# Performance work log

Measured on AMD Instinct MI355X. Metric: run time of the kernel, lower is better.

## Reference

```python
import jax, jax.numpy as jnp
import numpy as np

N_NODES = 50000
N_EDGES = 1600000
D_FEAT = 32
SCALE = 1.0
EPS = 1e-12


def setup_inputs() -> dict:
    key = jax.random.key(0)
    k1, k2 = jax.random.split(key)
    x = jax.random.normal(k1, (N_NODES, D_FEAT), dtype=jnp.float32)
    edge_index = jax.random.randint(k2, (2, N_EDGES), 0, N_NODES, dtype=jnp.int32)
    return {"x": x, "edge_index": edge_index}


def reference(x, edge_index):
    index_i = edge_index[0]  # target nodes (segments)
    index_j = edge_index[1]  # source nodes (gathered)

    # in-degree per target node, clamped to 1 (torch_scatter 'mean' semantics:
    # empty segments get mean 0)
    ones = jnp.ones((index_i.shape[0],), dtype=x.dtype)
    deg = jax.ops.segment_sum(ones, index_i, num_segments=N_NODES)
    deg = jnp.maximum(deg, 1.0)[:, None]  # [N, 1]

    # neighborhood mean of features
    mean = jax.ops.segment_sum(x[index_j], index_i, num_segments=N_NODES) / deg

    # neighborhood mean of squared deviations -> std
    reduced_x = (x - mean) ** 2
    var = jax.ops.segment_sum(reduced_x[index_j], index_i, num_segments=N_NODES) / deg
    std = jnp.sqrt(var + EPS)

    out = SCALE * x / std
    # replace infs with the original x, as in the torch module
    out = jnp.where(jnp.isinf(out), x, out)
    return out
```

## Files before the change

### kernel.cpp

```cpp
#include <hip/hip_runtime.h>
#include <hip/hip_fp16.h>
#include <math.h>

#define DF 32
#define EPSF 1e-12f
#define PB 128
#define PB_SHIFT 7
#define NBMAX 512
#define CAP 5120
#define CHUNK 4096
#define EPT 16

__global__ __launch_bounds__(256) void k_passA(
    const int* __restrict__ ii, const int* __restrict__ jj,
    const float* __restrict__ x, int* __restrict__ gcount,
    unsigned int* __restrict__ bucketed, __half* __restrict__ xh,
    int ne, int nb, int nfeat) {
  __shared__ int hist[NBMAX];
  __shared__ int histc[NBMAX];
  __shared__ int bb[NBMAX];
  __shared__ int excl_s[NBMAX];
  __shared__ int sc[256];
  __shared__ unsigned int stage[CHUNK];
  int t = threadIdx.x;
  hist[t] = 0; hist[t + 256] = 0;
  __syncthreads();

  int base = blockIdx.x * CHUNK;
  unsigned int pk[EPT];
  int rk[EPT];
#pragma unroll
  for (int k = 0; k < EPT; ++k) {
    int e = base + t + k * 256;
    if (e < ne) {
      int i = ii[e], j = jj[e];
      int b = i >> PB_SHIFT;
      pk[k] = ((unsigned)b << 23) | ((unsigned)(i & (PB - 1)) << 16) | (unsigned)j;
      rk[k] = atomicAdd(&hist[b], 1);
    } else {
      rk[k] = -1;
    }
  }

  {
    int base8 = blockIdx.x * (CHUNK / 8);
#pragma unroll
    for (int r = 0; r < 2; ++r) {
      int p8 = base8 + r * 256 + t;
      if (p8 * 8 < nfeat) {
        float4 a = ((const float4*)x)[2 * p8];
        float4 bq = ((const float4*)x)[2 * p8 + 1];
        union { __half2 h[4]; float4 f; } u;
        u.h[0] = __floats2half2_rn(a.x, a.y);
        u.h[1] = __floats2half2_rn(a.z, a.w);
        u.h[2] = __floats2half2_rn(bq.x, bq.y);
        u.h[3] = __floats2half2_rn(bq.z, bq.w);
        ((float4*)xh)[p8] = u.f;
      }
    }
  }
  __syncthreads();
  histc[t] = hist[t]; histc[t + 256] = hist[t + 256];
  __syncthreads();
#pragma unroll
  for (int b = t; b < NBMAX; b += 256) {
    int c = histc[b];
    bb[b] = (b < nb && c > 0) ? atomicAdd(&gcount[b], c) : 0;
  }
  int a0 = histc[2 * t], a1 = histc[2 * t + 1];
  sc[t] = a0 + a1;
  __syncthreads();
  int pv = sc[t];
  for (int s = 1; s < 256; s <<= 1) {
    int v = 0;
    if (t >= s) v = sc[t - s];
    __syncthreads();
    if (t >= s) sc[t] += v;
    __syncthreads();
  }
  int eP = sc[t] - pv;
  excl_s[2 * t] = eP;
  excl_s[2 * t + 1] = eP + a0;
  __syncthreads();
#pragma unroll
  for (int k = 0; k < EPT; ++k) {
    if (rk[k] >= 0) {
      int b = pk[k] >> 23;
      stage[excl_s[b] + rk[k]] = pk[k];
    }
  }
  __syncthreads();
  int bcnt = ne - base;
  if (bcnt > CHUNK) bcnt = CHUNK;
  for (int p = t; p < bcnt; p += 256) {
    unsigned int v = stage[p];
    int b = v >> 23;
    bucketed[(size_t)b * CAP + bb[b] + (p - excl_s[b])] = v;
  }
}

__global__ __launch_bounds__(256) void k_passB(
    const unsigned int* __restrict__ bucketed, const int* __restrict__ gcount,
    int* __restrict__ sortedj, int* __restrict__ deg_g, int* __restrict__ curend_g,
    int* __restrict__ perm, int n_nodes, int nb) {
  __shared__ int sc[256];
  __shared__ int lh[PB];
  __shared__ int lcur[PB];
  __shared__ int dh[PB];
  __shared__ int dcur[PB];
  __shared__ int sgbase;
  int b = blockIdx.x;
  int t = threadIdx.x;

  int g0 = (2 * t < nb) ? gcount[2 * t] : 0;
  int g1 = (2 * t + 1 < nb) ? gcount[2 * t + 1] : 0;
  sc[t] = g0 + g1;
  __syncthreads();
  int pv = sc[t];
  for (int s = 1; s < 256; s <<= 1) {
    int v = 0;
    if (t >= s) v = sc[t - s];
    __syncthreads();
    if (t >= s) sc[t] += v;
    __syncthreads();
  }
  if (2 * t == b) sgbase = sc[t] - pv;
  if (2 * t + 1 == b) sgbase = sc[t] - pv + g0;
  if (t < PB) { lh[t] = 0; dh[t] = 0; }
  __syncthreads();
  int gbase = sgbase;
  int cnt = gcount[b];

  const unsigned int* src = bucketed + (size_t)b * CAP;
  for (int p = t; p < cnt; p += 256) {
    int il = (src[p] >> 16) & (PB - 1);
    atomicAdd(&lh[il], 1);
  }
  __syncthreads();
  int a = (t < PB) ? lh[t] : 0;
  if (t < PB) sc[t] = a;
  __syncthreads();
  for (int s = 1; s < PB; s <<= 1) {
    int v = 0;
    if (t < PB && t >= s) v = sc[t - s];
    __syncthreads();
    if (t < PB && t >= s) sc[t] += v;
    __syncthreads();
  }
  int excl = (t < PB) ? sc[t] - a : 0;
  int node = b * PB + t;
  bool nvalid = (t < PB) && (node < n_nodes);
  if (t < PB) lcur[t] = excl;
  if (nvalid) {
    deg_g[node] = a;
    curend_g[node] = gbase + excl + a;
    atomicAdd(&dh[a < PB - 1 ? a : PB - 1], 1);
  }
  __syncthreads();
  int d0 = (t < PB) ? dh[t] : 0;
  if (t < PB) sc[t] = d0;
  __syncthreads();
  for (int s = 1; s < PB; s <<= 1) {
    int v = 0;
    if (t < PB && t >= s) v = sc[t - s];
    __syncthreads();
    if (t < PB && t >= s) sc[t] += v;
    __syncthreads();
  }
  if (t < PB) dcur[t] = sc[t] - d0;
  __syncthreads();
  if (nvalid) {
    int bin = a < PB - 1 ? a : PB - 1;
    int pos = atomicAdd(&dcur[bin], 1);
    perm[b * PB + pos] = node;
  } else if (t < PB) {
    perm[b * PB + t] = -1;
  }
  __syncthreads();
  for (int p = t; p < cnt; p += 256) {
    unsigned int v = src[p];
    int il = (v >> 16) & (PB - 1);
    int pos = atomicAdd(&lcur[il], 1);
    sortedj[gbase + pos] = (int)(v & 0xFFFFu);
  }
}

__global__ __launch_bounds__(256) void k_meansq(
    const int* __restrict__ perm, const int* __restrict__ sortedj,
    const int* __restrict__ curend, const int* __restrict__ deg,
    const __half* __restrict__ xh, const float* __restrict__ x,
    __half* __restrict__ yh, int nperm) {
  int wv = (int)((blockIdx.x * blockDim.x + threadIdx.x) >> 6);
  int lane = threadIdx.x & 63;
  int g = lane >> 3;
  int r = (lane >> 2) & 1;
  int c = lane & 3;
  int ni = wv * 8 + g;
  int w = perm[ni];
  bool valid = (w >= 0);
  int dg = valid ? deg[w] : 0;
  int end = valid ? curend[w] : 0;
  int start = end - dg;
  int co = c * 8;
  __half2 aA0 = {}, aA1 = {}, aA2 = {}, aA3 = {};
  __half2 aB0 = {}, aB1 = {}, aB2 = {}, aB3 = {};
  int s = start + r;
  for (; s + 6 < end; s += 8) {
    int j0 = sortedj[s], j1 = sortedj[s + 2], j2 = sortedj[s + 4], j3 = sortedj[s + 6];
    float4 v0 = *(const float4*)&xh[j0 * DF + co];
    float4 v1 = *(const float4*)&xh[j1 * DF + co];
    float4 v2 = *(const float4*)&xh[j2 * DF + co];
    float4 v3 = *(const float4*)&xh[j3 * DF + co];
    const __half2* h0 = (const __half2*)&v0;
    const __half2* h1 = (const __half2*)&v1;
    const __half2* h2 = (const __half2*)&v2;
    const __half2* h3 = (const __half2*)&v3;
    aA0 = __hadd2(aA0, h0[0]); aA1 = __hadd2(aA1, h0[1]);
    aA2 = __hadd2(aA2, h0[2]); aA3 = __hadd2(aA3, h0[3]);
    aB0 = __hadd2(aB0, h1[0]); aB1 = __hadd2(aB1, h1[1]);
    aB2 = __hadd2(aB2, h1[2]); aB3 = __hadd2(aB3, h1[3]);
    aA0 = __hadd2(aA0, h2[0]); aA1 = __hadd2(aA1, h2[1]);
    aA2 = __hadd2(aA2, h2[2]); aA3 = __hadd2(aA3, h2[3]);
    aB0 = __hadd2(aB0, h3[0]); aB1 = __hadd2(aB1, h3[1]);
    aB2 = __hadd2(aB2, h3[2]); aB3 = __hadd2(aB3, h3[3]);
  }
  for (; s < end; s += 2) {
    int j = sortedj[s];
    float4 v = *(const float4*)&xh[j * DF + co];
    const __half2* h = (const __half2*)&v;
    aA0 = __hadd2(aA0, h[0]); aA1 = __hadd2(aA1, h[1]);
    aA2 = __hadd2(aA2, h[2]); aA3 = __hadd2(aA3, h[3]);
  }
  __half2 s0 = __hadd2(aA0, aB0), s1 = __hadd2(aA1, aB1);
  __half2 s2 = __hadd2(aA2, aB2), s3 = __hadd2(aA3, aB3);
  union { __half2 h; int i; } u0, u1, u2, u3;
  u0.h = s0; u1.h = s1; u2.h = s2; u3.h = s3;
  u0.i = __shfl_xor(u0.i, 4); s0 = __hadd2(s0, u0.h);
  u1.i = __shfl_xor(u1.i, 4); s1 = __hadd2(s1, u1.h);
  u2.i = __shfl_xor(u2.i, 4); s2 = __hadd2(s2, u2.h);
  u3.i = __shfl_xor(u3.i, 4); s3 = __hadd2(s3, u3.h);
  if (valid && r == 0) {
    float inv = 1.0f / fmaxf((float)dg, 1.0f);
    float2 m0 = __half22float2(s0);
    float2 m1 = __half22float2(s1);
    float2 m2 = __half22float2(s2);
    float2 m3 = __half22float2(s3);
    float4 xa = *(const float4*)&x[w * DF + co];
    float4 xb = *(const float4*)&x[w * DF + co + 4];
    float d0 = xa.x - m0.x * inv;
    float d1 = xa.y - m0.y * inv;
    float d2 = xa.z - m1.x * inv;
    float d3 = xa.w - m1.y * inv;
    float d4 = xb.x - m2.x * inv;
    float d5 = xb.y - m2.y * inv;
    float d6 = xb.z - m3.x * inv;
    float d7 = xb.w - m3.y * inv;
    union { __half2 h[4]; float4 f; } uo;
    uo.h[0] = __floats2half2_rn(d0 * d0, d1 * d1);
    uo.h[1] = __floats2half2_rn(d2 * d2, d3 * d3);
    uo.h[2] = __floats2half2_rn(d4 * d4, d5 * d5);
    uo.h[3] = __floats2half2_rn(d6 * d6, d7 * d7);
    *(float4*)&yh[w * DF + co] = uo.f;
  }
}

__global__ __launch_bounds__(256) void k_varfinal(
    const int* __restrict__ perm, const int* __restrict__ sortedj,
    const int* __restrict__ curend, const int* __restrict__ deg,
    const __half* __restrict__ yh, const float* __restrict__ x,
    float* __restrict__ out, int nperm) {
  int wv = (int)((blockIdx.x * blockDim.x + threadIdx.x) >> 6);
  int lane = threadIdx.x & 63;
  int g = lane >> 3;
  int r = (lane >> 2) & 1;
  int c = lane & 3;
  int ni = wv * 8 + g;
  int w = perm[ni];
  bool valid = (w >= 0);
  int dg = valid ? deg[w] : 0;
  int end = valid ? curend[w] : 0;
  int start = end - dg;
  int co = c * 8;
  float accA[8], accB[8];
#pragma unroll
  for (int k = 0; k < 8; ++k) { accA[k] = 0.f; accB[k] = 0.f; }
  int s = start + r;
  for (; s + 6 < end; s += 8) {
    int j0 = sortedj[s], j1 = sortedj[s + 2], j2 = sortedj[s + 4], j3 = sortedj[s + 6];
    float4 v0 = *(const float4*)&yh[j0 * DF + co];
    float4 v1 = *(const float4*)&yh[j1 * DF + co];
    float4 v2 = *(const float4*)&yh[j2 * DF + co];
    float4 v3 = *(const float4*)&yh[j3 * DF + co];
    const __half2* h0 = (const __half2*)&v0;
    const __half2* h1 = (const __half2*)&v1;
    const __half2* h2 = (const __half2*)&v2;
    const __half2* h3 = (const __half2*)&v3;
#pragma unroll
    for (int k = 0; k < 4; ++k) {
      float2 f0 = __half22float2(h0[k]);
      float2 f1 = __half22float2(h1[k]);
      float2 f2 = __half22float2(h2[k]);
      float2 f3 = __half22float2(h3[k]);
      accA[2 * k]     += f0.x + f2.x;
      accA[2 * k + 1] += f0.y + f2.y;
      accB[2 * k]     += f1.x + f3.x;
      accB[2 * k + 1] += f1.y + f3.y;
    }
  }
  for (; s < end; s += 2) {
    int j = sortedj[s];
    float4 v = *(const float4*)&yh[j * DF + co];
    const __half2* h = (const __half2*)&v;
#pragma unroll
    for (int k = 0; k < 4; ++k) {
      float2 f = __half22float2(h[k]);
      accA[2 * k]     += f.x;
      accA[2 * k + 1] += f.y;
    }
  }
  float acc[8];
#pragma unroll
  for (int k = 0; k < 8; ++k) {
    acc[k] = accA[k] + accB[k];
    acc[k] += __shfl_xor(acc[k], 4);
  }
  if (valid && r == 0) {
    float dgc = fmaxf((float)dg, 1.0f);
    float4 xa = *(const float4*)&x[w * DF + co];
    float4 xb = *(const float4*)&x[w * DF + co + 4];
    float xs[8] = {xa.x, xa.y, xa.z, xa.w, xb.x, xb.y, xb.z, xb.w};
    float o[8];
#pragma unroll
    for (int k = 0; k < 8; ++k) {
      float sq = sqrtf(acc[k] / dgc + EPSF);
      o[k] = xs[k] / sq;
      if (isinf(o[k])) o[k] = xs[k];
    }
    float4 oa = {o[0], o[1], o[2], o[3]};
    float4 ob = {o[4], o[5], o[6], o[7]};
    *(float4*)&out[w * DF + co] = oa;
    *(float4*)&out[w * DF + co + 4] = ob;
  }
}

extern "C" void kernel_launch(void* const* d_in, const int* in_sizes, int n_in,
                              void* d_out, int out_size, void* d_ws, size_t ws_size,
                              hipStream_t stream) {
  const float* x = (const float*)d_in[0];
  const int* ei = (const int*)d_in[1];
  const int n_nodes = in_sizes[0] / DF;
  const int ne = in_sizes[1] / 2;
  const int* ii = ei;
  const int* jj = ei + ne;
  const int nb = (n_nodes + PB - 1) / PB;
  const int nfeat = n_nodes * DF;
  const int nperm = nb * PB;

  char* wsb = (char*)d_ws;
  size_t off = 0;
  auto align16 = [](size_t v) { return (v + 15) & ~(size_t)15; };
  int* gcount = (int*)(wsb + off); off = align16(off + NBMAX * 4);
  int* deg    = (int*)(wsb + off); off = align16(off + (size_t)n_nodes * 4);
  int* curend = (int*)(wsb + off); off = align16(off + (size_t)n_nodes * 4);
  int* perm   = (int*)(wsb + off); off = align16(off + (size_t)nperm * 4);
  int* sortedj= (int*)(wsb + off); off = align16(off + (size_t)ne * 4);
  unsigned int* bucketed = (unsigned int*)(wsb + off);
  off = align16(off + (size_t)nb * CAP * 4);
  __half* xh = (__half*)(wsb + off); off = align16(off + (size_t)nfeat * 2);
  __half* yh = (__half*)(wsb + off);

  float* out = (float*)d_out;

  hipMemsetAsync(gcount, 0, NBMAX * sizeof(int), stream);

  int nblkA = (ne + CHUNK - 1) / CHUNK;
  int nblkF = (nfeat + CHUNK - 1) / CHUNK;
  if (nblkF > nblkA) nblkA = nblkF;
  k_passA<<<nblkA, 256, 0, stream>>>(ii, jj, x, gcount, bucketed, xh, ne, nb, nfeat);
  k_passB<<<nb, 256, 0, stream>>>(bucketed, gcount, sortedj, deg, curend, perm, n_nodes, nb);

  int gblocks = nperm / 32;
  k_meansq<<<gblocks, 256, 0, stream>>>(perm, sortedj, curend, deg, xh, x, yh, nperm);
  k_varfinal<<<gblocks, 256, 0, stream>>>(perm, sortedj, curend, deg, yh, x, out, nperm);
}
```

Before: 85.77 us.

## Drop LDS staging in bucketing pass and write scattered directly with smaller chunks

Pass A no longer sorts each chunk's packed edges into a shared-memory staging buffer with a block-wide prefix scan before writing them out. Each edge is now written straight to its global bucket slot from registers. The chunk size is halved so twice as many blocks run, each with less work and much less shared memory. This removes the scan, several barriers and the LDS round trip, at the cost of less coalesced global writes and twice as many global atomics on the bucket counters.

```diff
diff --git a/kernel.cpp b/kernel.cpp
--- a/kernel.cpp
+++ b/kernel.cpp
@@ -8,8 +8,8 @@
 #define PB_SHIFT 7
 #define NBMAX 512
 #define CAP 5120
-#define CHUNK 4096
-#define EPT 16
+#define CHUNK 2048
+#define EPT 8
 
 __global__ __launch_bounds__(256) void k_passA(
     const int* __restrict__ ii, const int* __restrict__ jj,
@@ -17,11 +17,7 @@
     unsigned int* __restrict__ bucketed, __half* __restrict__ xh,
     int ne, int nb, int nfeat) {
   __shared__ int hist[NBMAX];
-  __shared__ int histc[NBMAX];
   __shared__ int bb[NBMAX];
-  __shared__ int excl_s[NBMAX];
-  __shared__ int sc[256];
-  __shared__ unsigned int stage[CHUNK];
   int t = threadIdx.x;
   hist[t] = 0; hist[t + 256] = 0;
   __syncthreads();
@@ -43,59 +39,31 @@
   }
 
   {
-    int base8 = blockIdx.x * (CHUNK / 8);
-#pragma unroll
-    for (int r = 0; r < 2; ++r) {
-      int p8 = base8 + r * 256 + t;
-      if (p8 * 8 < nfeat) {
-        float4 a = ((const float4*)x)[2 * p8];
-        float4 bq = ((const float4*)x)[2 * p8 + 1];
-        union { __half2 h[4]; float4 f; } u;
-        u.h[0] = __floats2half2_rn(a.x, a.y);
-        u.h[1] = __floats2half2_rn(a.z, a.w);
-        u.h[2] = __floats2half2_rn(bq.x, bq.y);
-        u.h[3] = __floats2half2_rn(bq.z, bq.w);
-        ((float4*)xh)[p8] = u.f;
-      }
-    }
-  }
-  __syncthreads();
-  histc[t] = hist[t]; histc[t + 256] = hist[t + 256];
+    int p8 = blockIdx.x * (CHUNK / 8) + t;
+    if (p8 * 8 < nfeat) {
+      float4 a = ((const float4*)x)[2 * p8];
+      float4 bq = ((const float4*)x)[2 * p8 + 1];
+      union { __half2 h[4]; float4 f; } u;
+      u.h[0] = __floats2half2_rn(a.x, a.y);
+      u.h[1] = __floats2half2_rn(a.z, a.w);
+      u.h[2] = __floats2half2_rn(bq.x, bq.y);
+      u.h[3] = __floats2half2_rn(bq.z, bq.w);
+      ((float4*)xh)[p8] = u.f;
+    }
+  }
   __syncthreads();
 #pragma unroll
   for (int b = t; b < NBMAX; b += 256) {
-    int c = histc[b];
+    int c = hist[b];
     bb[b] = (b < nb && c > 0) ? atomicAdd(&gcount[b], c) : 0;
   }
-  int a0 = histc[2 * t], a1 = histc[2 * t + 1];
-  sc[t] = a0 + a1;
-  __syncthreads();
-  int pv = sc[t];
-  for (int s = 1; s < 256; s <<= 1) {
-    int v = 0;
-    if (t >= s) v = sc[t - s];
-    __syncthreads();
-    if (t >= s) sc[t] += v;
-    __syncthreads();
-  }
-  int eP = sc[t] - pv;
-  excl_s[2 * t] = eP;
-  excl_s[2 * t + 1] = eP + a0;
   __syncthreads();
 #pragma unroll
   for (int k = 0; k < EPT; ++k) {
     if (rk[k] >= 0) {
       int b = pk[k] >> 23;
-      stage[excl_s[b] + rk[k]] = pk[k];
-    }
-  }
-  __syncthreads();
-  int bcnt = ne - base;
-  if (bcnt > CHUNK) bcnt = CHUNK;
-  for (int p = t; p < bcnt; p += 256) {
-    unsigned int v = stage[p];
-    int b = v >> 23;
-    bucketed[(size_t)b * CAP + bb[b] + (p - excl_s[b])] = v;
+      bucketed[(size_t)b * CAP + bb[b] + rk[k]] = pk[k];
+    }
   }
 }
 
```

Result: slower. 97.42 us (+13.6%).

## Fuse bucket sort with neighbor-mean pass and store sorted indices as ushort

Applied to the files above, without the earlier changes.

Merges the per-bucket counting sort kernel with the mean and squared-deviation gather kernel. The sorted source indices are kept in LDS and the mean is computed in the same block, which removes one kernel launch and the global round-trip of the sorted index list for the mean pass. The global sorted index array also shrinks to 16-bit entries for the variance pass. In exchange, the gather now runs in only one block per 128-node bucket rather than many small blocks, so there are fewer waves in flight to hide gather latency, and the larger LDS footprint may lower occupancy.

```diff
diff --git a/kernel.cpp b/kernel.cpp
--- a/kernel.cpp
+++ b/kernel.cpp
@@ -95,22 +95,28 @@
   for (int p = t; p < bcnt; p += 256) {
     unsigned int v = stage[p];
     int b = v >> 23;
-    bucketed[(size_t)b * CAP + bb[b] + (p - excl_s[b])] = v;
+    int excl = excl_s[b];
+    bucketed[(size_t)b * CAP + bb[b] + (p - excl)] = v;
   }
 }
 
-__global__ __launch_bounds__(256) void k_passB(
+__global__ __launch_bounds__(256) void k_sortmean(
     const unsigned int* __restrict__ bucketed, const int* __restrict__ gcount,
-    int* __restrict__ sortedj, int* __restrict__ deg_g, int* __restrict__ curend_g,
-    int* __restrict__ perm, int n_nodes, int nb) {
+    const __half* __restrict__ xh, const float* __restrict__ x,
+    __half* __restrict__ yh, unsigned short* __restrict__ sortedj,
+    int* __restrict__ deg_g, int* __restrict__ curend_g, int* __restrict__ perm,
+    int n_nodes, int nb) {
   __shared__ int sc[256];
   __shared__ int lh[PB];
   __shared__ int lcur[PB];
   __shared__ int dh[PB];
   __shared__ int dcur[PB];
+  __shared__ int nstart[PB];
+  __shared__ int ndeg[PB];
+  __shared__ int npl[PB];
+  __shared__ unsigned short sjl[CAP];
   __shared__ int sgbase;
-  int b = blockIdx.x;
-  int t = threadIdx.x;
+  int b = blockIdx.x, t = threadIdx.x;
 
   int g0 = (2 * t < nb) ? gcount[2 * t] : 0;
   int g1 = (2 * t + 1 < nb) ? gcount[2 * t + 1] : 0;
@@ -130,12 +136,9 @@
   __syncthreads();
   int gbase = sgbase;
   int cnt = gcount[b];
-
   const unsigned int* src = bucketed + (size_t)b * CAP;
-  for (int p = t; p < cnt; p += 256) {
-    int il = (src[p] >> 16) & (PB - 1);
-    atomicAdd(&lh[il], 1);
-  }
+
+  for (int p = t; p < cnt; p += 256) atomicAdd(&lh[(src[p] >> 16) & (PB - 1)], 1);
   __syncthreads();
   int a = (t < PB) ? lh[t] : 0;
   if (t < PB) sc[t] = a;
@@ -150,7 +153,7 @@
   int excl = (t < PB) ? sc[t] - a : 0;
   int node = b * PB + t;
   bool nvalid = (t < PB) && (node < n_nodes);
-  if (t < PB) lcur[t] = excl;
+  if (t < PB) { lcur[t] = excl; nstart[t] = excl; ndeg[t] = a; }
   if (nvalid) {
     deg_g[node] = a;
     curend_g[node] = gbase + excl + a;
@@ -172,8 +175,10 @@
   if (nvalid) {
     int bin = a < PB - 1 ? a : PB - 1;
     int pos = atomicAdd(&dcur[bin], 1);
+    npl[pos] = t;
     perm[b * PB + pos] = node;
   } else if (t < PB) {
+    npl[t] = -1;
     perm[b * PB + t] = -1;
   }
   __syncthreads();
@@ -181,91 +186,88 @@
     unsigned int v = src[p];
     int il = (v >> 16) & (PB - 1);
     int pos = atomicAdd(&lcur[il], 1);
-    sortedj[gbase + pos] = (int)(v & 0xFFFFu);
+    sjl[pos] = (unsigned short)(v & 0xFFFFu);
+  }
+  __syncthreads();
+  for (int p = t; p < cnt; p += 256) sortedj[gbase + p] = sjl[p];
+
+  int wvl = t >> 6, lane = t & 63;
+  int g = lane >> 3, r = (lane >> 2) & 1, c = lane & 3;
+  int co = c * 8;
+#pragma unroll
+  for (int sweep = 0; sweep < PB / 32; ++sweep) {
+    int slot = sweep * 32 + wvl * 8 + g;
+    int il = npl[slot];
+    bool valid = (il >= 0);
+    int dg = valid ? ndeg[il] : 0;
+    int st = valid ? nstart[il] : 0;
+    int en = st + dg;
+    __half2 aA0 = {}, aA1 = {}, aA2 = {}, aA3 = {};
+    __half2 aB0 = {}, aB1 = {}, aB2 = {}, aB3 = {};
+    int s = st + r;
+    for (; s + 6 < en; s += 8) {
+      int j0 = sjl[s], j1 = sjl[s + 2], j2 = sjl[s + 4], j3 = sjl[s + 6];
+      float4 v0 = *(const float4*)&xh[j0 * DF + co];
+      float4 v1 = *(const float4*)&xh[j1 * DF + co];
+      float4 v2 = *(const float4*)&xh[j2 * DF + co];
+      float4 v3 = *(const float4*)&xh[j3 * DF + co];
+      const __half2* h0 = (const __half2*)&v0;
+      const __half2* h1 = (const __half2*)&v1;
+      const __half2* h2 = (const __half2*)&v2;
+      const __half2* h3 = (const __half2*)&v3;
+      aA0 = __hadd2(aA0, h0[0]); aA1 = __hadd2(aA1, h0[1]);
+      aA2 = __hadd2(aA2, h0[2]); aA3 = __hadd2(aA3, h0[3]);
+      aB0 = __hadd2(aB0, h1[0]); aB1 = __hadd2(aB1, h1[1]);
+      aB2 = __hadd2(aB2, h1[2]); aB3 = __hadd2(aB3, h1[3]);
+      aA0 = __hadd2(aA0, h2[0]); aA1 = __hadd2(aA1, h2[1]);
+      aA2 = __hadd2(aA2, h2[2]); aA3 = __hadd2(aA3, h2[3]);
+      aB0 = __hadd2(aB0, h3[0]); aB1 = __hadd2(aB1, h3[1]);
+      aB2 = __hadd2(aB2, h3[2]); aB3 = __hadd2(aB3, h3[3]);
+    }
+    for (; s < en; s += 2) {
+      int j = sjl[s];
+      float4 v = *(const float4*)&xh[j * DF + co];
+      const __half2* h = (const __half2*)&v;
+      aA0 = __hadd2(aA0, h[0]); aA1 = __hadd2(aA1, h[1]);
+      aA2 = __hadd2(aA2, h[2]); aA3 = __hadd2(aA3, h[3]);
+    }
+    __half2 s0 = __hadd2(aA0, aB0), s1 = __hadd2(aA1, aB1);
+    __half2 s2 = __hadd2(aA2, aB2), s3 = __hadd2(aA3, aB3);
+    union { __half2 h; int i; } u0, u1, u2, u3;
+    u0.h = s0; u1.h = s1; u2.h = s2; u3.h = s3;
+    u0.i = __shfl_xor(u0.i, 4); s0 = __hadd2(s0, u0.h);
+    u1.i = __shfl_xor(u1.i, 4); s1 = __hadd2(s1, u1.h);
+    u2.i = __shfl_xor(u2.i, 4); s2 = __hadd2(s2, u2.h);
+    u3.i = __shfl_xor(u3.i, 4); s3 = __hadd2(s3, u3.h);
+    if (valid && r == 0) {
+      int w = b * PB + il;
+      float inv = 1.0f / fmaxf((float)dg, 1.0f);
+      float2 m0 = __half22float2(s0);
+      float2 m1 = __half22float2(s1);
+      float2 m2 = __half22float2(s2);
+      float2 m3 = __half22float2(s3);
+      float4 xa = *(const float4*)&x[w * DF + co];
+      float4 xb = *(const float4*)&x[w * DF + co + 4];
+      float d0 = xa.x - m0.x * inv;
+      float d1 = xa.y - m0.y * inv;
+      float d2 = xa.z - m1.x * inv;
+      float d3 = xa.w - m1.y * inv;
+      float d4 = xb.x - m2.x * inv;
+      float d5 = xb.y - m2.y * inv;
+      float d6 = xb.z - m3.x * inv;
+      float d7 = xb.w - m3.y * inv;
+      union { __half2 h[4]; float4 f; } uo;
+      uo.h[0] = __floats2half2_rn(d0 * d0, d1 * d1);
+      uo.h[1] = __floats2half2_rn(d2 * d2, d3 * d3);
+      uo.h[2] = __floats2half2_rn(d4 * d4, d5 * d5);
+      uo.h[3] = __floats2half2_rn(d6 * d6, d7 * d7);
+      *(float4*)&yh[w * DF + co] = uo.f;
+    }
   }
 }
 
-__global__ __launch_bounds__(256) void k_meansq(
-    const int* __restrict__ perm, const int* __restrict__ sortedj,
-    const int* __restrict__ curend, const int* __restrict__ deg,
-    const __half* __restrict__ xh, const float* __restrict__ x,
-    __half* __restrict__ yh, int nperm) {
-  int wv = (int)((blockIdx.x * blockDim.x + threadIdx.x) >> 6);
-  int lane = threadIdx.x & 63;
-  int g = lane >> 3;
-  int r = (lane >> 2) & 1;
-  int c = lane & 3;
-  int ni = wv * 8 + g;
-  int w = perm[ni];
-  bool valid = (w >= 0);
-  int dg = valid ? deg[w] : 0;
-  int end = valid ? curend[w] : 0;
-  int start = end - dg;
-  int co = c * 8;
-  __half2 aA0 = {}, aA1 = {}, aA2 = {}, aA3 = {};
-  __half2 aB0 = {}, aB1 = {}, aB2 = {}, aB3 = {};
-  int s = start + r;
-  for (; s + 6 < end; s += 8) {
-    int j0 = sortedj[s], j1 = sortedj[s + 2], j2 = sortedj[s + 4], j3 = sortedj[s + 6];
-    float4 v0 = *(const float4*)&xh[j0 * DF + co];
-    float4 v1 = *(const float4*)&xh[j1 * DF + co];
-    float4 v2 = *(const float4*)&xh[j2 * DF + co];
-    float4 v3 = *(const float4*)&xh[j3 * DF + co];
-    const __half2* h0 = (const __half2*)&v0;
-    const __half2* h1 = (const __half2*)&v1;
-    const __half2* h2 = (const __half2*)&v2;
-    const __half2* h3 = (const __half2*)&v3;
-    aA0 = __hadd2(aA0, h0[0]); aA1 = __hadd2(aA1, h0[1]);
-    aA2 = __hadd2(aA2, h0[2]); aA3 = __hadd2(aA3, h0[3]);
-    aB0 = __hadd2(aB0, h1[0]); aB1 = __hadd2(aB1, h1[1]);
-    aB2 = __hadd2(aB2, h1[2]); aB3 = __hadd2(aB3, h1[3]);
-    aA0 = __hadd2(aA0, h2[0]); aA1 = __hadd2(aA1, h2[1]);
-    aA2 = __hadd2(aA2, h2[2]); aA3 = __hadd2(aA3, h2[3]);
-    aB0 = __hadd2(aB0, h3[0]); aB1 = __hadd2(aB1, h3[1]);
-    aB2 = __hadd2(aB2, h3[2]); aB3 = __hadd2(aB3, h3[3]);
-  }
-  for (; s < end; s += 2) {
-    int j = sortedj[s];
-    float4 v = *(const float4*)&xh[j * DF + co];
-    const __half2* h = (const __half2*)&v;
-    aA0 = __hadd2(aA0, h[0]); aA1 = __hadd2(aA1, h[1]);
-    aA2 = __hadd2(aA2, h[2]); aA3 = __hadd2(aA3, h[3]);
-  }
-  __half2 s0 = __hadd2(aA0, aB0), s1 = __hadd2(aA1, aB1);
-  __half2 s2 = __hadd2(aA2, aB2), s3 = __hadd2(aA3, aB3);
-  union { __half2 h; int i; } u0, u1, u2, u3;
-  u0.h = s0; u1.h = s1; u2.h = s2; u3.h = s3;
-  u0.i = __shfl_xor(u0.i, 4); s0 = __hadd2(s0, u0.h);
-  u1.i = __shfl_xor(u1.i, 4); s1 = __hadd2(s1, u1.h);
-  u2.i = __shfl_xor(u2.i, 4); s2 = __hadd2(s2, u2.h);
-  u3.i = __shfl_xor(u3.i, 4); s3 = __hadd2(s3, u3.h);
-  if (valid && r == 0) {
-    float inv = 1.0f / fmaxf((float)dg, 1.0f);
-    float2 m0 = __half22float2(s0);
-    float2 m1 = __half22float2(s1);
-    float2 m2 = __half22float2(s2);
-    float2 m3 = __half22float2(s3);
-    float4 xa = *(const float4*)&x[w * DF + co];
-    float4 xb = *(const float4*)&x[w * DF + co + 4];
-    float d0 = xa.x - m0.x * inv;
-    float d1 = xa.y - m0.y * inv;
-    float d2 = xa.z - m1.x * inv;
-    float d3 = xa.w - m1.y * inv;
-    float d4 = xb.x - m2.x * inv;
-    float d5 = xb.y - m2.y * inv;
-    float d6 = xb.z - m3.x * inv;
-    float d7 = xb.w - m3.y * inv;
-    union { __half2 h[4]; float4 f; } uo;
-    uo.h[0] = __floats2half2_rn(d0 * d0, d1 * d1);
-    uo.h[1] = __floats2half2_rn(d2 * d2, d3 * d3);
-    uo.h[2] = __floats2half2_rn(d4 * d4, d5 * d5);
-    uo.h[3] = __floats2half2_rn(d6 * d6, d7 * d7);
-    *(float4*)&yh[w * DF + co] = uo.f;
-  }
-}
-
 __global__ __launch_bounds__(256) void k_varfinal(
-    const int* __restrict__ perm, const int* __restrict__ sortedj,
+    const int* __restrict__ perm, const unsigned short* __restrict__ sortedj,
     const int* __restrict__ curend, const int* __restrict__ deg,
     const __half* __restrict__ yh, const float* __restrict__ x,
     float* __restrict__ out, int nperm) {
@@ -363,7 +365,8 @@
   int* deg    = (int*)(wsb + off); off = align16(off + (size_t)n_nodes * 4);
   int* curend = (int*)(wsb + off); off = align16(off + (size_t)n_nodes * 4);
   int* perm   = (int*)(wsb + off); off = align16(off + (size_t)nperm * 4);
-  int* sortedj= (int*)(wsb + off); off = align16(off + (size_t)ne * 4);
+  unsigned short* sortedj = (unsigned short*)(wsb + off);
+  off = align16(off + (size_t)ne * 2);
   unsigned int* bucketed = (unsigned int*)(wsb + off);
   off = align16(off + (size_t)nb * CAP * 4);
   __half* xh = (__half*)(wsb + off); off = align16(off + (size_t)nfeat * 2);
@@ -377,9 +380,9 @@
   int nblkF = (nfeat + CHUNK - 1) / CHUNK;
   if (nblkF > nblkA) nblkA = nblkF;
   k_passA<<<nblkA, 256, 0, stream>>>(ii, jj, x, gcount, bucketed, xh, ne, nb, nfeat);
-  k_passB<<<nb, 256, 0, stream>>>(bucketed, gcount, sortedj, deg, curend, perm, n_nodes, nb);
+  k_sortmean<<<nb, 256, 0, stream>>>(bucketed, gcount, xh, x, yh, sortedj,
+                                     deg, curend, perm, n_nodes, nb);
 
   int gblocks = nperm / 32;
-  k_meansq<<<gblocks, 256, 0, stream>>>(perm, sortedj, curend, deg, xh, x, yh, nperm);
   k_varfinal<<<gblocks, 256, 0, stream>>>(perm, sortedj, curend, deg, yh, x, out, nperm);
 }
```

Result: faster. 75.72 us (-11.7%).
